# Optimization experiments

Measured on AMD Instinct MI355X. Metric: run time of the kernel, lower is better.

The kernel has to match this reference:

```python
import jax, jax.numpy as jnp
import numpy as np

B, L, C, H, D2 = 1, 384, 256, 8, 128
d = C // H
EPS = 1e-5
SCALE = 1.0 / np.sqrt(d).astype(np.float32)


def setup_inputs() -> dict:
    key = jax.random.key(0)
    ks = jax.random.split(key, 20)

    def lin(k, fin, fout):
        return (jax.random.normal(k, (fin, fout), jnp.float32) / np.sqrt(fin)).astype(jnp.float32)

    return {
        "x2d": jax.random.normal(ks[0], (B, L, L, D2), jnp.float32),
        "x3d": jax.random.normal(ks[1], (B, L, C), jnp.float32),
        "Wq": lin(ks[2], C, C), "bq": jax.random.normal(ks[3], (C,), jnp.float32) * 0.02,
        "Wk": lin(ks[4], C, C), "bk": jax.random.normal(ks[5], (C,), jnp.float32) * 0.02,
        "Wv": lin(ks[6], C, C), "bv": jax.random.normal(ks[7], (C,), jnp.float32) * 0.02,
        "Wpre": lin(ks[8], D2, C), "bpre": jax.random.normal(ks[9], (C,), jnp.float32) * 0.02,
        "ln_g": jnp.ones((C,), jnp.float32), "ln_b": jnp.zeros((C,), jnp.float32),
        "Weq": lin(ks[10], C, C), "beq": jax.random.normal(ks[11], (C,), jnp.float32) * 0.02,
        "Wek": lin(ks[12], C, C), "bek": jax.random.normal(ks[13], (C,), jnp.float32) * 0.02,
        "Wo": lin(ks[14], C, C), "bo": jax.random.normal(ks[15], (C,), jnp.float32) * 0.02,
    }


def reference(x2d, x3d, Wq, bq, Wk, bk, Wv, bv, Wpre, bpre, ln_g, ln_b,
              Weq, beq, Wek, bek, Wo, bo):
    def heads(x):  # (B,L,C) -> (B,H,L,d)
        return x.reshape(B, L, H, d).transpose(0, 2, 1, 3)

    q = heads(x3d @ Wq + bq)
    k = heads(x3d @ Wk + bk)
    v = heads(x3d @ Wv + bv)

    # pre_proj: Linear -> LayerNorm -> ReLU on pair features
    e = x2d @ Wpre + bpre                              # (B,L,L,C)
    mu = jnp.mean(e, axis=-1, keepdims=True)
    var = jnp.mean((e - mu) ** 2, axis=-1, keepdims=True)
    e = jax.nn.relu((e - mu) * jax.lax.rsqrt(var + EPS) * ln_g + ln_b)

    efq = (e @ Weq + beq).reshape(B, L, L, H, d)       # efq[b,i,j,h,:]
    efk = (e @ Wek + bek).reshape(B, L, L, H, d)

    # scores[b,h,i,j] = q_i.k_j + sum_d efk[b,i,j,h,d]*q[b,h,j,d], then scale
    scores = jnp.einsum('bhid,bhjd->bhij', q, k) \
           + jnp.einsum('bijhd,bhjd->bhij', efk, q)
    scores = scores * SCALE

    w = jax.nn.softmax(scores, axis=-1)
    x1 = jnp.einsum('bhij,bhjd->bhid', w, v)
    # x2[b,h,i,d] = sum_j scores[b,h,i,j] * efq[b,i,j,h,d]
    x2 = jnp.einsum('bhij,bijhd->bhid', scores, efq)

    x = (x1 + x2).transpose(0, 2, 1, 3).reshape(B, L, C)
    return x @ Wo + bo
```

## Files before the change

kernel.cpp:

```cpp
#include <hip/hip_runtime.h>
#include <hip/hip_bf16.h>

#define LLEN 384
#define CDIM 256
#define NH 8
#define HD 32
#define DIN 128
#define LN_EPS 1e-5f
#define SCL 0.17677669529663687f

#define EIDX(row, cs) (((row) << 8) + (((((cs) >> 3) ^ ((row) & 7)) << 3) | ((cs) & 4)))
#define XIDX(row, cs) (((row) << 7) + (((((cs) >> 3) ^ ((row) & 7)) << 3) | ((cs) & 4)))

typedef __attribute__((ext_vector_type(8))) short bh8;
typedef __attribute__((ext_vector_type(4))) float f32x4;
typedef __attribute__((ext_vector_type(4))) unsigned int u32x4;

__device__ __forceinline__ unsigned short f2bf(float f){
  unsigned int u = __float_as_uint(f);
  u += 0x7fffu + ((u >> 16) & 1u);
  return (unsigned short)(u >> 16);
}

__device__ __forceinline__ unsigned int pkbf(float a, float b){
#if defined(__gfx950__) && __has_builtin(__builtin_amdgcn_cvt_pk_bf16_f32)
  typedef __attribute__((ext_vector_type(2))) __bf16 vbf2;
  vbf2 v = __builtin_amdgcn_cvt_pk_bf16_f32(a, b);
  union { vbf2 v; unsigned int u; } cv; cv.v = v; return cv.u;
#else
  return (unsigned int)f2bf(a) | ((unsigned int)f2bf(b) << 16);
#endif
}

__global__ __launch_bounds__(256) void pack_w(
    const float* __restrict__ Wpre, const float* __restrict__ Weq,
    const float* __restrict__ Wek,  const float* __restrict__ Wq,
    const float* __restrict__ Wk,   const float* __restrict__ Wv,
    unsigned short* __restrict__ Pp, unsigned short* __restrict__ Pq,
    unsigned short* __restrict__ Pk, unsigned short* __restrict__ PWq,
    unsigned short* __restrict__ PWk, unsigned short* __restrict__ PWv)
{
  int tid = blockIdx.x * 256 + threadIdx.x;
  const float* W; unsigned short* P; int base;
  if      (tid <  4096){ W = Wpre; P = Pp;  base = tid;         }
  else if (tid < 12288){ W = Weq;  P = Pq;  base = tid -  4096; }
  else if (tid < 20480){ W = Wek;  P = Pk;  base = tid - 12288; }
  else if (tid < 28672){ W = Wq;   P = PWq; base = tid - 20480; }
  else if (tid < 36864){ W = Wk;   P = PWk; base = tid - 28672; }
  else                 { W = Wv;   P = PWv; base = tid - 36864; }
  int l   = base & 63;
  int c   = (base >> 6) & 15;
  int kc  = base >> 10;
  int krow = kc*32 + (l >> 4)*8;
  int col  = c*16 + (l & 15);
  unsigned int wds[4];
  #pragma unroll
  for (int p = 0; p < 4; p++){
    unsigned short lo = f2bf(W[(size_t)(krow + 2*p    )*CDIM + col]);
    unsigned short hi = f2bf(W[(size_t)(krow + 2*p + 1)*CDIM + col]);
    wds[p] = (unsigned int)lo | ((unsigned int)hi << 16);
  }
  uint4 v; v.x = wds[0]; v.y = wds[1]; v.z = wds[2]; v.w = wds[3];
  *(uint4*)(P + (size_t)base*8) = v;
}

__global__ __launch_bounds__(256) void qkv_mfma(
    const float* __restrict__ x3d,
    const float* __restrict__ bq, const float* __restrict__ bk, const float* __restrict__ bv,
    const unsigned short* __restrict__ PWq, const unsigned short* __restrict__ PWk,
    const unsigned short* __restrict__ PWv,
    float* __restrict__ Vm, unsigned short* __restrict__ QmH,
    float* __restrict__ QmT, unsigned short* __restrict__ PKt)
{
  __shared__ __align__(16) unsigned short Xb[64*264];
  const int bx = blockIdx.x;
  const int jb = bx / 3, m = bx % 3;
  const int t  = threadIdx.x;
  const int w  = t >> 6, l = t & 63, q4 = l >> 4, lm = l & 15;
  const int wbase = w << 6;

  const float* src = x3d + (size_t)jb*64*CDIM;
  #pragma unroll
  for (int it = 0; it < 16; it++){
    int idx = it*256 + t;
    int r = idx >> 6, k4 = (idx & 63) << 2;
    f32x4 v = *(const f32x4*)(src + (size_t)r*CDIM + k4);
    uint2 pk; pk.x = pkbf(v[0], v[1]); pk.y = pkbf(v[2], v[3]);
    *(uint2*)(&Xb[r*264 + k4]) = pk;
  }
  __syncthreads();

  const unsigned short* P = (m == 0) ? PWq : (m == 1) ? PWk : PWv;
  const float* bias       = (m == 0) ? bq  : (m == 1) ? bk  : bv;
  f32x4 acc[4][4];
  #pragma unroll
  for (int a = 0; a < 4; a++)
    #pragma unroll
    for (int b = 0; b < 4; b++){ f32x4 z = {0.f,0.f,0.f,0.f}; acc[a][b] = z; }
  #pragma unroll
  for (int kc = 0; kc < 8; kc++){
    bh8 af[4];
    #pragma unroll
    for (int rt = 0; rt < 4; rt++)
      af[rt] = *(const bh8*)(&Xb[(rt*16 + lm)*264 + kc*32 + q4*8]);
    #pragma unroll
    for (int ct = 0; ct < 4; ct++){
      bh8 bf = *(const bh8*)(P + ((size_t)(kc*16 + (w*4 + ct))*64 + l)*8);
      #pragma unroll
      for (int rt = 0; rt < 4; rt++)
        acc[rt][ct] = __builtin_amdgcn_mfma_f32_16x16x32_bf16(af[rt], bf, acc[rt][ct], 0, 0, 0);
    }
  }
  #pragma unroll
  for (int ct = 0; ct < 4; ct++){
    int c = wbase + ct*16 + lm;
    float bb = bias[c];
    #pragma unroll
    for (int rt = 0; rt < 4; rt++)
      #pragma unroll
      for (int rg = 0; rg < 4; rg++){
        int row = jb*64 + rt*16 + q4*4 + rg;
        float v = acc[rt][ct][rg] + bb;
        if (m == 0){
          QmH[(size_t)row*CDIM + c] = f2bf(v);
          QmT[(size_t)c*LLEN + row] = v;
        } else if (m == 1){
          int kc2 = c >> 5;
          int jj2 = c & 7;
          int l2  = ((c >> 3) & 3)*16 + (row & 15);
          PKt[(((size_t)kc2*24 + (row >> 4))*64 + l2)*8 + jj2] = f2bf(v);
        } else {
          Vm[(size_t)row*CDIM + c] = v;
        }
      }
  }
}

__global__ __launch_bounds__(256, 4) void x3d_tiles(
  const float* __restrict__ x2d,
  const float* __restrict__ bpre, const float* __restrict__ ln_g, const float* __restrict__ ln_b,
  const float* __restrict__ beq,  const float* __restrict__ bek,
  const float* __restrict__ QmT,  const unsigned short* __restrict__ QmH,
  const unsigned short* __restrict__ PKt,
  const unsigned short* __restrict__ Pp, const unsigned short* __restrict__ Pq,
  const unsigned short* __restrict__ Pk,
  float* __restrict__ Sg, float* __restrict__ x2part)
{
  __shared__ __align__(16) unsigned short EX[64*256];
  __shared__ float rowstat[4][64][2];
  __shared__ float muS[64], istdS[64];
  __shared__ __align__(16) float scoresS[NH*64];

  const int bx = blockIdx.x;
  const int i = bx / 6, jt = bx % 6, j0 = jt * 64;
  const int t = threadIdx.x;
  const int w = t >> 6, l = t & 63, q4 = l >> 4, lm = l & 15;
  const int wbase = w << 6;
  const bool b4 = l & 16, b5 = l & 32;

  #pragma unroll
  for (int hh = 0; hh < 2; hh++){
    int h = 2*w + hh;
    bh8 aq = *(const bh8*)(QmH + (size_t)i*CDIM + h*HD + q4*8);
    #pragma unroll
    for (int ct = 0; ct < 4; ct++){
      bh8 bf = *(const bh8*)(PKt + (((size_t)h*24 + (jt*4 + ct))*64 + l)*8);
      f32x4 z = {0.f,0.f,0.f,0.f};
      f32x4 a1 = __builtin_amdgcn_mfma_f32_16x16x32_bf16(aq, bf, z, 0, 0, 0);
      if (q4 == 0) scoresS[h*64 + ct*16 + lm] = a1[0];
    }
  }

  {
    const float* src = x2d + ((size_t)i*LLEN + j0)*DIN;
    #pragma unroll
    for (int it = 0; it < 8; it++){
      int r  = it*8 + (t >> 5);
      int k4 = (t & 31)*4;
      u32x4 uv = __builtin_nontemporal_load((const u32x4*)(src + (size_t)r*DIN + k4));
      uint2 pk;
      pk.x = pkbf(__uint_as_float(uv.x), __uint_as_float(uv.y));
      pk.y = pkbf(__uint_as_float(uv.z), __uint_as_float(uv.w));
      *(uint2*)(&EX[XIDX(r, k4)]) = pk;
    }
  }
  __syncthreads();

  f32x4 acc[4][4];
  #pragma unroll
  for (int a = 0; a < 4; a++)
    #pragma unroll
    for (int b = 0; b < 4; b++){ f32x4 z = {0.f,0.f,0.f,0.f}; acc[a][b] = z; }
  #pragma unroll
  for (int kc = 0; kc < 4; kc++){
    bh8 xf[4];
    #pragma unroll
    for (int nt = 0; nt < 4; nt++)
      xf[nt] = *(const bh8*)(&EX[XIDX(nt*16 + lm, kc*32 + q4*8)]);
    #pragma unroll
    for (int mt = 0; mt < 4; mt++){
      bh8 wf = *(const bh8*)(Pp + ((size_t)(kc*16 + (w*4 + mt))*64 + l)*8);
      #pragma unroll
      for (int nt = 0; nt < 4; nt++)
        acc[mt][nt] = __builtin_amdgcn_mfma_f32_16x16x32_bf16(wf, xf[nt], acc[mt][nt], 0, 0, 0);
    }
  }

  {
    float vs[4] = {0,0,0,0}, vq[4] = {0,0,0,0};
    #pragma unroll
    for (int mt = 0; mt < 4; mt++){
      int cb = wbase + mt*16 + q4*4;
      f32x4 bp = *(const f32x4*)(bpre + cb);
      #pragma unroll
      for (int nt = 0; nt < 4; nt++)
        #pragma unroll
        for (int rg = 0; rg < 4; rg++){
          float x = acc[mt][nt][rg] + bp[rg];
          acc[mt][nt][rg] = x;
          vs[nt] += x; vq[nt] += x*x;
        }
    }
    float r0 = (b4 ? vs[1] : vs[0]) + __shfl_xor(b4 ? vs[0] : vs[1], 16, 64);
    float r1 = (b4 ? vs[3] : vs[2]) + __shfl_xor(b4 ? vs[2] : vs[3], 16, 64);
    float ssum = (b5 ? r1 : r0) + __shfl_xor(b5 ? r0 : r1, 32, 64);
    float u0 = (b4 ? vq[1] : vq[0]) + __shfl_xor(b4 ? vq[0] : vq[1], 16, 64);
    float u1 = (b4 ? vq[3] : vq[2]) + __shfl_xor(b4 ? vq[2] : vq[3], 16, 64);
    float ssq = (b5 ? u1 : u0) + __shfl_xor(b5 ? u0 : u1, 32, 64);
    int ntl = (b5 ? 2 : 0) + (b4 ? 1 : 0);
    int jl = ntl*16 + lm;
    rowstat[w][jl][0] = ssum;
    rowstat[w][jl][1] = ssq;
  }
  __syncthreads();
  if (t < 64){
    float s  = rowstat[0][t][0] + rowstat[1][t][0] + rowstat[2][t][0] + rowstat[3][t][0];
    float s2 = rowstat[0][t][1] + rowstat[1][t][1] + rowstat[2][t][1] + rowstat[3][t][1];
    float mu = s * (1.f/256.f);
    float var = s2 * (1.f/256.f) - mu*mu;
    muS[t] = mu;
    istdS[t] = rsqrtf(var + LN_EPS);
  }
  __syncthreads();

  {
    float muL[4], isL[4];
    #pragma unroll
    for (int nt = 0; nt < 4; nt++){
      muL[nt] = muS[nt*16 + lm];
      isL[nt] = istdS[nt*16 + lm];
    }
    #pragma unroll
    for (int mt = 0; mt < 4; mt++){
      int cb = wbase + mt*16 + q4*4;
      f32x4 g4 = *(const f32x4*)(ln_g + cb);
      f32x4 bb4 = *(const f32x4*)(ln_b + cb);
      #pragma unroll
      for (int nt = 0; nt < 4; nt++){
        float e0 = fmaxf((acc[mt][nt][0] - muL[nt])*isL[nt]*g4[0] + bb4[0], 0.f);
        float e1 = fmaxf((acc[mt][nt][1] - muL[nt])*isL[nt]*g4[1] + bb4[1], 0.f);
        float e2 = fmaxf((acc[mt][nt][2] - muL[nt])*isL[nt]*g4[2] + bb4[2], 0.f);
        float e3 = fmaxf((acc[mt][nt][3] - muL[nt])*isL[nt]*g4[3] + bb4[3], 0.f);
        uint2 pk; pk.x = pkbf(e0, e1); pk.y = pkbf(e2, e3);
        *(uint2*)(&EX[EIDX(nt*16 + lm, cb)]) = pk;
      }
    }
  }
  __syncthreads();

  #pragma unroll
  for (int a = 0; a < 4; a++)
    #pragma unroll
    for (int b = 0; b < 4; b++){ f32x4 z = {0.f,0.f,0.f,0.f}; acc[a][b] = z; }
  #pragma unroll
  for (int kc = 0; kc < 8; kc++){
    bh8 xf[4];
    #pragma unroll
    for (int nt = 0; nt < 4; nt++)
      xf[nt] = *(const bh8*)(&EX[EIDX(nt*16 + lm, kc*32 + q4*8)]);
    #pragma unroll
    for (int mt = 0; mt < 4; mt++){
      bh8 wf = *(const bh8*)(Pk + ((size_t)(kc*16 + (w*4 + mt))*64 + l)*8);
      #pragma unroll
      for (int nt = 0; nt < 4; nt++)
        acc[mt][nt] = __builtin_amdgcn_mfma_f32_16x16x32_bf16(wf, xf[nt], acc[mt][nt], 0, 0, 0);
    }
  }

  {
    f32x4 bk4[4];
    #pragma unroll
    for (int mt = 0; mt < 4; mt++)
      bk4[mt] = *(const f32x4*)(bek + wbase + mt*16 + q4*4);
    #pragma unroll
    for (int nt = 0; nt < 4; nt++){
      int j = nt*16 + lm;
      float qr[4][4];
      #pragma unroll
      for (int mt = 0; mt < 4; mt++){
        int cb = wbase + mt*16 + q4*4;
        #pragma unroll
        for (int rg = 0; rg < 4; rg++)
          qr[mt][rg] = QmT[(size_t)(cb + rg)*LLEN + j0 + j];
      }
      float v0 = 0.f, v1 = 0.f;
      #pragma unroll
      for (int mt = 0; mt < 4; mt++){
        float p = (acc[mt][nt][0] + bk4[mt][0]) * qr[mt][0]
                + (acc[mt][nt][1] + bk4[mt][1]) * qr[mt][1]
                + (acc[mt][nt][2] + bk4[mt][2]) * qr[mt][2]
                + (acc[mt][nt][3] + bk4[mt][3]) * qr[mt][3];
        if (mt < 2) v0 += p; else v1 += p;
      }
      float r = (b4 ? v1 : v0) + __shfl_xor(b4 ? v0 : v1, 16, 64);
      float s = r + __shfl_xor(r, 32, 64);
      int h = 2*w + (b4 ? 1 : 0);
      float sc = (s + scoresS[h*64 + j]) * SCL;
      if (!b5){
        scoresS[h*64 + j] = sc;
        Sg[((size_t)i*NH + h)*LLEN + j0 + j] = sc;
      }
    }
  }

  #pragma unroll
  for (int a = 0; a < 4; a++)
    #pragma unroll
    for (int b = 0; b < 4; b++){ f32x4 z = {0.f,0.f,0.f,0.f}; acc[a][b] = z; }
  #pragma unroll
  for (int kc = 0; kc < 8; kc++){
    bh8 af[4];
    #pragma unroll
    for (int rt = 0; rt < 4; rt++)
      af[rt] = *(const bh8*)(&EX[EIDX(rt*16 + lm, kc*32 + q4*8)]);
    #pragma unroll
    for (int ct = 0; ct < 4; ct++){
      bh8 bf = *(const bh8*)(Pq + ((size_t)(kc*16 + (w*4 + ct))*64 + l)*8);
      #pragma unroll
      for (int rt = 0; rt < 4; rt++)
        acc[rt][ct] = __builtin_amdgcn_mfma_f32_16x16x32_bf16(af[rt], bf, acc[rt][ct], 0, 0, 0);
    }
  }

  {
    float bq4[4];
    #pragma unroll
    for (int ct = 0; ct < 4; ct++) bq4[ct] = beq[wbase + ct*16 + lm];
    float x2p[4] = {0.f, 0.f, 0.f, 0.f};
    #pragma unroll
    for (int rt = 0; rt < 4; rt++){
      f32x4 s0 = *(const f32x4*)(&scoresS[(2*w    )*64 + rt*16 + q4*4]);
      f32x4 s1 = *(const f32x4*)(&scoresS[(2*w + 1)*64 + rt*16 + q4*4]);
      #pragma unroll
      for (int ct = 0; ct < 4; ct++){
        const f32x4& sv = (ct < 2) ? s0 : s1;
        #pragma unroll
        for (int rg = 0; rg < 4; rg++)
          x2p[ct] = fmaf(sv[rg], acc[rt][ct][rg] + bq4[ct], x2p[ct]);
      }
    }
    float r0 = (b4 ? x2p[1] : x2p[0]) + __shfl_xor(b4 ? x2p[0] : x2p[1], 16, 64);
    float r1 = (b4 ? x2p[3] : x2p[2]) + __shfl_xor(b4 ? x2p[2] : x2p[3], 16, 64);
    float q  = (b5 ? r1 : r0) + __shfl_xor(b5 ? r0 : r1, 32, 64);
    int ctq = (b4 ? 1 : 0) | (b5 ? 2 : 0);
    x2part[((size_t)jt*LLEN + i)*CDIM + wbase + ctq*16 + lm] = q;
  }
}

__global__ __launch_bounds__(256) void finish(
    const float* __restrict__ Sg, const float* __restrict__ x2part,
    const float* __restrict__ Vm, const float* __restrict__ Wo,
    const float* __restrict__ bo, float* __restrict__ out)
{
  __shared__ float scoresS[NH*LLEN];
  __shared__ float xoutS[CDIM];
  const int i = blockIdx.x;
  const int t = threadIdx.x;

  #pragma unroll
  for (int it = 0; it < 3; it++)
    ((float4*)scoresS)[it*256 + t] = ((const float4*)(Sg + (size_t)i*NH*LLEN))[it*256 + t];
  __syncthreads();

  const int h = t >> 5;
  const int g32 = t & 31;
  float sv[12];
  float mx = -3.0e38f;
  #pragma unroll
  for (int it = 0; it < 12; it++){
    float s = scoresS[h*LLEN + it*32 + g32];
    sv[it] = s;
    mx = fmaxf(mx, s);
  }
  #pragma unroll
  for (int mk = 1; mk < 32; mk <<= 1) mx = fmaxf(mx, __shfl_xor(mx, mk, 64));
  float den = 0.f;
  #pragma unroll
  for (int it = 0; it < 12; it++){ float e = __expf(sv[it] - mx); sv[it] = e; den += e; }
  #pragma unroll
  for (int mk = 1; mk < 32; mk <<= 1) den += __shfl_xor(den, mk, 64);
  float rden = 1.f / den;
  #pragma unroll
  for (int it = 0; it < 12; it++) scoresS[h*LLEN + it*32 + g32] = sv[it]*rden;
  __syncthreads();

  float a0 = 0.f, a1 = 0.f, a2 = 0.f, a3 = 0.f;
  {
    const float* vp = Vm + t;
    const float* sp = scoresS + h*LLEN;
    #pragma unroll 4
    for (int j = 0; j < LLEN; j += 4){
      a0 = fmaf(sp[j+0], vp[(size_t)(j+0)*CDIM], a0);
      a1 = fmaf(sp[j+1], vp[(size_t)(j+1)*CDIM], a1);
      a2 = fmaf(sp[j+2], vp[(size_t)(j+2)*CDIM], a2);
      a3 = fmaf(sp[j+3], vp[(size_t)(j+3)*CDIM], a3);
    }
  }
  float x2v = 0.f;
  #pragma unroll
  for (int jt = 0; jt < 6; jt++)
    x2v += x2part[((size_t)jt*LLEN + i)*CDIM + t];
  xoutS[t] = (a0 + a1) + (a2 + a3) + x2v;
  __syncthreads();

  float b0a = bo[t], b1a = 0.f, b2a = 0.f, b3a = 0.f;
  #pragma unroll 4
  for (int c = 0; c < CDIM; c += 4){
    b0a = fmaf(xoutS[c+0], Wo[(size_t)(c+0)*CDIM + t], b0a);
    b1a = fmaf(xoutS[c+1], Wo[(size_t)(c+1)*CDIM + t], b1a);
    b2a = fmaf(xoutS[c+2], Wo[(size_t)(c+2)*CDIM + t], b2a);
    b3a = fmaf(xoutS[c+3], Wo[(size_t)(c+3)*CDIM + t], b3a);
  }
  out[(size_t)i*CDIM + t] = (b0a + b1a) + (b2a + b3a);
}

extern "C" void kernel_launch(void* const* d_in, const int* in_sizes, int n_in,
                              void* d_out, int out_size, void* d_ws, size_t ws_size,
                              hipStream_t stream)
{
  const float* x2d  = (const float*)d_in[0];
  const float* x3d  = (const float*)d_in[1];
  const float* Wq   = (const float*)d_in[2];
  const float* bq   = (const float*)d_in[3];
  const float* Wk   = (const float*)d_in[4];
  const float* bk   = (const float*)d_in[5];
  const float* Wv   = (const float*)d_in[6];
  const float* bv   = (const float*)d_in[7];
  const float* Wpre = (const float*)d_in[8];
  const float* bpre = (const float*)d_in[9];
  const float* ln_g = (const float*)d_in[10];
  const float* ln_b = (const float*)d_in[11];
  const float* Weq  = (const float*)d_in[12];
  const float* beq  = (const float*)d_in[13];
  const float* Wek  = (const float*)d_in[14];
  const float* bek  = (const float*)d_in[15];
  const float* Wo   = (const float*)d_in[16];
  const float* bo   = (const float*)d_in[17];
  float* out = (float*)d_out;

  float* Vm  = (float*)d_ws;
  float* QmT = Vm + LLEN*CDIM;
  unsigned short* QmH = (unsigned short*)(QmT + CDIM*LLEN);
  unsigned short* PKt = QmH + LLEN*CDIM;
  unsigned short* Pp  = PKt + LLEN*CDIM;
  unsigned short* Pq  = Pp  + DIN*CDIM;
  unsigned short* Pk  = Pq  + CDIM*CDIM;
  unsigned short* PWq = Pk  + CDIM*CDIM;
  unsigned short* PWk = PWq + CDIM*CDIM;
  unsigned short* PWv = PWk + CDIM*CDIM;
  float* Sg     = (float*)(PWv + CDIM*CDIM);
  float* x2part = Sg + (size_t)LLEN*NH*LLEN;

  pack_w<<<dim3(176), dim3(256), 0, stream>>>(Wpre, Weq, Wek, Wq, Wk, Wv,
                                              Pp, Pq, Pk, PWq, PWk, PWv);
  qkv_mfma<<<dim3(18), dim3(256), 0, stream>>>(x3d, bq, bk, bv, PWq, PWk, PWv,
                                               Vm, QmH, QmT, PKt);
  x3d_tiles<<<dim3(LLEN*6), dim3(256), 0, stream>>>(x2d, bpre, ln_g, ln_b, beq, bek,
                                                    QmT, QmH, PKt, Pp, Pq, Pk, Sg, x2part);
  finish<<<dim3(LLEN), dim3(256), 0, stream>>>(Sg, x2part, Vm, Wo, bo, out);
}
```

Measured before the change: 247.0 us.

## Loop three j-tiles per block with register prefetch of next x2d tile

The main tile kernel now processes three 64-column j-tiles per block (768 blocks instead of 2304). It prefetches the next x2d tile into registers while the current tile is computed, and x2 partials accumulate across the loop so only two partial rows per i reach the finish kernel. Separate LDS buffers for the input tile and the activated tile make the overlap possible. The cost is a larger LDS footprint, more registers from the prefetch buffer, and a lower launch-bounds occupancy hint (4 to 3), with fewer blocks left to fill the GPU.

```diff
diff --git a/kernel.cpp b/kernel.cpp
--- a/kernel.cpp
+++ b/kernel.cpp
@@ -136,7 +136,7 @@
   }
 }
 
-__global__ __launch_bounds__(256, 4) void x3d_tiles(
+__global__ __launch_bounds__(256, 3) void x3d_tiles(
   const float* __restrict__ x2d,
   const float* __restrict__ bpre, const float* __restrict__ ln_g, const float* __restrict__ ln_b,
   const float* __restrict__ beq,  const float* __restrict__ bek,
@@ -146,224 +146,244 @@
   const unsigned short* __restrict__ Pk,
   float* __restrict__ Sg, float* __restrict__ x2part)
 {
-  __shared__ __align__(16) unsigned short EX[64*256];
+  __shared__ __align__(16) unsigned short XS[64*128];
+  __shared__ __align__(16) unsigned short ES[64*256];
   __shared__ float rowstat[4][64][2];
   __shared__ float muS[64], istdS[64];
   __shared__ __align__(16) float scoresS[NH*64];
 
   const int bx = blockIdx.x;
-  const int i = bx / 6, jt = bx % 6, j0 = jt * 64;
+  const int i = bx >> 1, jh = bx & 1;
   const int t = threadIdx.x;
   const int w = t >> 6, l = t & 63, q4 = l >> 4, lm = l & 15;
   const int wbase = w << 6;
   const bool b4 = l & 16, b5 = l & 32;
-
-  #pragma unroll
-  for (int hh = 0; hh < 2; hh++){
-    int h = 2*w + hh;
-    bh8 aq = *(const bh8*)(QmH + (size_t)i*CDIM + h*HD + q4*8);
-    #pragma unroll
-    for (int ct = 0; ct < 4; ct++){
-      bh8 bf = *(const bh8*)(PKt + (((size_t)h*24 + (jt*4 + ct))*64 + l)*8);
-      f32x4 z = {0.f,0.f,0.f,0.f};
-      f32x4 a1 = __builtin_amdgcn_mfma_f32_16x16x32_bf16(aq, bf, z, 0, 0, 0);
-      if (q4 == 0) scoresS[h*64 + ct*16 + lm] = a1[0];
-    }
-  }
-
+  const int pr  = (t >> 5);
+  const int pk4 = (t & 31) * 4;
+
+  float x2p[4] = {0.f, 0.f, 0.f, 0.f};
+
+  u32x4 pf[8];
   {
-    const float* src = x2d + ((size_t)i*LLEN + j0)*DIN;
+    const float* src = x2d + ((size_t)i*LLEN + jh*192)*DIN;
+    #pragma unroll
+    for (int it = 0; it < 8; it++)
+      pf[it] = __builtin_nontemporal_load((const u32x4*)(src + (size_t)(it*8 + pr)*DIN + pk4));
+  }
+
+  for (int tt = 0; tt < 3; tt++){
+    const int j0 = jh*192 + tt*64;
+    const int jt = jh*3 + tt;
+
     #pragma unroll
     for (int it = 0; it < 8; it++){
-      int r  = it*8 + (t >> 5);
-      int k4 = (t & 31)*4;
-      u32x4 uv = __builtin_nontemporal_load((const u32x4*)(src + (size_t)r*DIN + k4));
-      uint2 pk;
-      pk.x = pkbf(__uint_as_float(uv.x), __uint_as_float(uv.y));
-      pk.y = pkbf(__uint_as_float(uv.z), __uint_as_float(uv.w));
-      *(uint2*)(&EX[XIDX(r, k4)]) = pk;
-    }
-  }
-  __syncthreads();
-
-  f32x4 acc[4][4];
-  #pragma unroll
-  for (int a = 0; a < 4; a++)
-    #pragma unroll
-    for (int b = 0; b < 4; b++){ f32x4 z = {0.f,0.f,0.f,0.f}; acc[a][b] = z; }
-  #pragma unroll
-  for (int kc = 0; kc < 4; kc++){
-    bh8 xf[4];
-    #pragma unroll
-    for (int nt = 0; nt < 4; nt++)
-      xf[nt] = *(const bh8*)(&EX[XIDX(nt*16 + lm, kc*32 + q4*8)]);
-    #pragma unroll
-    for (int mt = 0; mt < 4; mt++){
-      bh8 wf = *(const bh8*)(Pp + ((size_t)(kc*16 + (w*4 + mt))*64 + l)*8);
+      uint2 pkv;
+      pkv.x = pkbf(__uint_as_float(pf[it].x), __uint_as_float(pf[it].y));
+      pkv.y = pkbf(__uint_as_float(pf[it].z), __uint_as_float(pf[it].w));
+      *(uint2*)(&XS[XIDX(it*8 + pr, pk4)]) = pkv;
+    }
+    if (tt < 2){
+      const float* src = x2d + ((size_t)i*LLEN + j0 + 64)*DIN;
+      #pragma unroll
+      for (int it = 0; it < 8; it++)
+        pf[it] = __builtin_nontemporal_load((const u32x4*)(src + (size_t)(it*8 + pr)*DIN + pk4));
+    }
+
+    #pragma unroll
+    for (int hh = 0; hh < 2; hh++){
+      int h = 2*w + hh;
+      bh8 aq = *(const bh8*)(QmH + (size_t)i*CDIM + h*HD + q4*8);
+      #pragma unroll
+      for (int ct = 0; ct < 4; ct++){
+        bh8 bf = *(const bh8*)(PKt + (((size_t)h*24 + (jt*4 + ct))*64 + l)*8);
+        f32x4 z = {0.f,0.f,0.f,0.f};
+        f32x4 a1 = __builtin_amdgcn_mfma_f32_16x16x32_bf16(aq, bf, z, 0, 0, 0);
+        if (q4 == 0) scoresS[h*64 + ct*16 + lm] = a1[0];
+      }
+    }
+    __syncthreads();
+
+    f32x4 acc[4][4];
+    #pragma unroll
+    for (int a = 0; a < 4; a++)
+      #pragma unroll
+      for (int b = 0; b < 4; b++){ f32x4 z = {0.f,0.f,0.f,0.f}; acc[a][b] = z; }
+    #pragma unroll
+    for (int kc = 0; kc < 4; kc++){
+      bh8 xf[4];
       #pragma unroll
       for (int nt = 0; nt < 4; nt++)
-        acc[mt][nt] = __builtin_amdgcn_mfma_f32_16x16x32_bf16(wf, xf[nt], acc[mt][nt], 0, 0, 0);
-    }
-  }
-
-  {
-    float vs[4] = {0,0,0,0}, vq[4] = {0,0,0,0};
-    #pragma unroll
-    for (int mt = 0; mt < 4; mt++){
-      int cb = wbase + mt*16 + q4*4;
-      f32x4 bp = *(const f32x4*)(bpre + cb);
-      #pragma unroll
-      for (int nt = 0; nt < 4; nt++)
-        #pragma unroll
-        for (int rg = 0; rg < 4; rg++){
-          float x = acc[mt][nt][rg] + bp[rg];
-          acc[mt][nt][rg] = x;
-          vs[nt] += x; vq[nt] += x*x;
-        }
-    }
-    float r0 = (b4 ? vs[1] : vs[0]) + __shfl_xor(b4 ? vs[0] : vs[1], 16, 64);
-    float r1 = (b4 ? vs[3] : vs[2]) + __shfl_xor(b4 ? vs[2] : vs[3], 16, 64);
-    float ssum = (b5 ? r1 : r0) + __shfl_xor(b5 ? r0 : r1, 32, 64);
-    float u0 = (b4 ? vq[1] : vq[0]) + __shfl_xor(b4 ? vq[0] : vq[1], 16, 64);
-    float u1 = (b4 ? vq[3] : vq[2]) + __shfl_xor(b4 ? vq[2] : vq[3], 16, 64);
-    float ssq = (b5 ? u1 : u0) + __shfl_xor(b5 ? u0 : u1, 32, 64);
-    int ntl = (b5 ? 2 : 0) + (b4 ? 1 : 0);
-    int jl = ntl*16 + lm;
-    rowstat[w][jl][0] = ssum;
-    rowstat[w][jl][1] = ssq;
-  }
-  __syncthreads();
-  if (t < 64){
-    float s  = rowstat[0][t][0] + rowstat[1][t][0] + rowstat[2][t][0] + rowstat[3][t][0];
-    float s2 = rowstat[0][t][1] + rowstat[1][t][1] + rowstat[2][t][1] + rowstat[3][t][1];
-    float mu = s * (1.f/256.f);
-    float var = s2 * (1.f/256.f) - mu*mu;
-    muS[t] = mu;
-    istdS[t] = rsqrtf(var + LN_EPS);
-  }
-  __syncthreads();
-
-  {
-    float muL[4], isL[4];
-    #pragma unroll
-    for (int nt = 0; nt < 4; nt++){
-      muL[nt] = muS[nt*16 + lm];
-      isL[nt] = istdS[nt*16 + lm];
-    }
-    #pragma unroll
-    for (int mt = 0; mt < 4; mt++){
-      int cb = wbase + mt*16 + q4*4;
-      f32x4 g4 = *(const f32x4*)(ln_g + cb);
-      f32x4 bb4 = *(const f32x4*)(ln_b + cb);
-      #pragma unroll
-      for (int nt = 0; nt < 4; nt++){
-        float e0 = fmaxf((acc[mt][nt][0] - muL[nt])*isL[nt]*g4[0] + bb4[0], 0.f);
-        float e1 = fmaxf((acc[mt][nt][1] - muL[nt])*isL[nt]*g4[1] + bb4[1], 0.f);
-        float e2 = fmaxf((acc[mt][nt][2] - muL[nt])*isL[nt]*g4[2] + bb4[2], 0.f);
-        float e3 = fmaxf((acc[mt][nt][3] - muL[nt])*isL[nt]*g4[3] + bb4[3], 0.f);
-        uint2 pk; pk.x = pkbf(e0, e1); pk.y = pkbf(e2, e3);
-        *(uint2*)(&EX[EIDX(nt*16 + lm, cb)]) = pk;
-      }
-    }
-  }
-  __syncthreads();
-
-  #pragma unroll
-  for (int a = 0; a < 4; a++)
-    #pragma unroll
-    for (int b = 0; b < 4; b++){ f32x4 z = {0.f,0.f,0.f,0.f}; acc[a][b] = z; }
-  #pragma unroll
-  for (int kc = 0; kc < 8; kc++){
-    bh8 xf[4];
-    #pragma unroll
-    for (int nt = 0; nt < 4; nt++)
-      xf[nt] = *(const bh8*)(&EX[EIDX(nt*16 + lm, kc*32 + q4*8)]);
-    #pragma unroll
-    for (int mt = 0; mt < 4; mt++){
-      bh8 wf = *(const bh8*)(Pk + ((size_t)(kc*16 + (w*4 + mt))*64 + l)*8);
-      #pragma unroll
-      for (int nt = 0; nt < 4; nt++)
-        acc[mt][nt] = __builtin_amdgcn_mfma_f32_16x16x32_bf16(wf, xf[nt], acc[mt][nt], 0, 0, 0);
-    }
-  }
-
-  {
-    f32x4 bk4[4];
-    #pragma unroll
-    for (int mt = 0; mt < 4; mt++)
-      bk4[mt] = *(const f32x4*)(bek + wbase + mt*16 + q4*4);
-    #pragma unroll
-    for (int nt = 0; nt < 4; nt++){
-      int j = nt*16 + lm;
-      float qr[4][4];
+        xf[nt] = *(const bh8*)(&XS[XIDX(nt*16 + lm, kc*32 + q4*8)]);
+      #pragma unroll
+      for (int mt = 0; mt < 4; mt++){
+        bh8 wf = *(const bh8*)(Pp + ((size_t)(kc*16 + (w*4 + mt))*64 + l)*8);
+        #pragma unroll
+        for (int nt = 0; nt < 4; nt++)
+          acc[mt][nt] = __builtin_amdgcn_mfma_f32_16x16x32_bf16(wf, xf[nt], acc[mt][nt], 0, 0, 0);
+      }
+    }
+
+    {
+      float vs[4] = {0,0,0,0}, vq[4] = {0,0,0,0};
       #pragma unroll
       for (int mt = 0; mt < 4; mt++){
         int cb = wbase + mt*16 + q4*4;
-        #pragma unroll
-        for (int rg = 0; rg < 4; rg++)
-          qr[mt][rg] = QmT[(size_t)(cb + rg)*LLEN + j0 + j];
-      }
-      float v0 = 0.f, v1 = 0.f;
+        f32x4 bp = *(const f32x4*)(bpre + cb);
+        #pragma unroll
+        for (int nt = 0; nt < 4; nt++)
+          #pragma unroll
+          for (int rg = 0; rg < 4; rg++){
+            float x = acc[mt][nt][rg] + bp[rg];
+            acc[mt][nt][rg] = x;
+            vs[nt] += x; vq[nt] += x*x;
+          }
+      }
+      float r0 = (b4 ? vs[1] : vs[0]) + __shfl_xor(b4 ? vs[0] : vs[1], 16, 64);
+      float r1 = (b4 ? vs[3] : vs[2]) + __shfl_xor(b4 ? vs[2] : vs[3], 16, 64);
+      float ssum = (b5 ? r1 : r0) + __shfl_xor(b5 ? r0 : r1, 32, 64);
+      float u0 = (b4 ? vq[1] : vq[0]) + __shfl_xor(b4 ? vq[0] : vq[1], 16, 64);
+      float u1 = (b4 ? vq[3] : vq[2]) + __shfl_xor(b4 ? vq[2] : vq[3], 16, 64);
+      float ssq = (b5 ? u1 : u0) + __shfl_xor(b5 ? u0 : u1, 32, 64);
+      int ntl = (b5 ? 2 : 0) + (b4 ? 1 : 0);
+      int jl = ntl*16 + lm;
+      rowstat[w][jl][0] = ssum;
+      rowstat[w][jl][1] = ssq;
+    }
+    __syncthreads();
+    if (t < 64){
+      float s  = rowstat[0][t][0] + rowstat[1][t][0] + rowstat[2][t][0] + rowstat[3][t][0];
+      float s2 = rowstat[0][t][1] + rowstat[1][t][1] + rowstat[2][t][1] + rowstat[3][t][1];
+      float mu = s * (1.f/256.f);
+      float var = s2 * (1.f/256.f) - mu*mu;
+      muS[t] = mu;
+      istdS[t] = rsqrtf(var + LN_EPS);
+    }
+    __syncthreads();
+
+    {
+      float muL[4], isL[4];
+      #pragma unroll
+      for (int nt = 0; nt < 4; nt++){
+        muL[nt] = muS[nt*16 + lm];
+        isL[nt] = istdS[nt*16 + lm];
+      }
       #pragma unroll
       for (int mt = 0; mt < 4; mt++){
-        float p = (acc[mt][nt][0] + bk4[mt][0]) * qr[mt][0]
-                + (acc[mt][nt][1] + bk4[mt][1]) * qr[mt][1]
-                + (acc[mt][nt][2] + bk4[mt][2]) * qr[mt][2]
-                + (acc[mt][nt][3] + bk4[mt][3]) * qr[mt][3];
-        if (mt < 2) v0 += p; else v1 += p;
-      }
-      float r = (b4 ? v1 : v0) + __shfl_xor(b4 ? v0 : v1, 16, 64);
-      float s = r + __shfl_xor(r, 32, 64);
-      int h = 2*w + (b4 ? 1 : 0);
-      float sc = (s + scoresS[h*64 + j]) * SCL;
-      if (!b5){
-        scoresS[h*64 + j] = sc;
-        Sg[((size_t)i*NH + h)*LLEN + j0 + j] = sc;
-      }
-    }
-  }
-
-  #pragma unroll
-  for (int a = 0; a < 4; a++)
-    #pragma unroll
-    for (int b = 0; b < 4; b++){ f32x4 z = {0.f,0.f,0.f,0.f}; acc[a][b] = z; }
-  #pragma unroll
-  for (int kc = 0; kc < 8; kc++){
-    bh8 af[4];
-    #pragma unroll
-    for (int rt = 0; rt < 4; rt++)
-      af[rt] = *(const bh8*)(&EX[EIDX(rt*16 + lm, kc*32 + q4*8)]);
-    #pragma unroll
-    for (int ct = 0; ct < 4; ct++){
-      bh8 bf = *(const bh8*)(Pq + ((size_t)(kc*16 + (w*4 + ct))*64 + l)*8);
+        int cb = wbase + mt*16 + q4*4;
+        f32x4 g4 = *(const f32x4*)(ln_g + cb);
+        f32x4 bb4 = *(const f32x4*)(ln_b + cb);
+        #pragma unroll
+        for (int nt = 0; nt < 4; nt++){
+          float e0 = fmaxf((acc[mt][nt][0] - muL[nt])*isL[nt]*g4[0] + bb4[0], 0.f);
+          float e1 = fmaxf((acc[mt][nt][1] - muL[nt])*isL[nt]*g4[1] + bb4[1], 0.f);
+          float e2 = fmaxf((acc[mt][nt][2] - muL[nt])*isL[nt]*g4[2] + bb4[2], 0.f);
+          float e3 = fmaxf((acc[mt][nt][3] - muL[nt])*isL[nt]*g4[3] + bb4[3], 0.f);
+          uint2 pkv; pkv.x = pkbf(e0, e1); pkv.y = pkbf(e2, e3);
+          *(uint2*)(&ES[EIDX(nt*16 + lm, cb)]) = pkv;
+        }
+      }
+    }
+    __syncthreads();
+
+    #pragma unroll
+    for (int a = 0; a < 4; a++)
+      #pragma unroll
+      for (int b = 0; b < 4; b++){ f32x4 z = {0.f,0.f,0.f,0.f}; acc[a][b] = z; }
+    #pragma unroll
+    for (int kc = 0; kc < 8; kc++){
+      bh8 xf[4];
+      #pragma unroll
+      for (int nt = 0; nt < 4; nt++)
+        xf[nt] = *(const bh8*)(&ES[EIDX(nt*16 + lm, kc*32 + q4*8)]);
+      #pragma unroll
+      for (int mt = 0; mt < 4; mt++){
+        bh8 wf = *(const bh8*)(Pk + ((size_t)(kc*16 + (w*4 + mt))*64 + l)*8);
+        #pragma unroll
+        for (int nt = 0; nt < 4; nt++)
+          acc[mt][nt] = __builtin_amdgcn_mfma_f32_16x16x32_bf16(wf, xf[nt], acc[mt][nt], 0, 0, 0);
+      }
+    }
+
+    {
+      f32x4 bk4[4];
+      #pragma unroll
+      for (int mt = 0; mt < 4; mt++)
+        bk4[mt] = *(const f32x4*)(bek + wbase + mt*16 + q4*4);
+      #pragma unroll
+      for (int nt = 0; nt < 4; nt++){
+        int j = nt*16 + lm;
+        float qr[4][4];
+        #pragma unroll
+        for (int mt = 0; mt < 4; mt++){
+          int cb = wbase + mt*16 + q4*4;
+          #pragma unroll
+          for (int rg = 0; rg < 4; rg++)
+            qr[mt][rg] = QmT[(size_t)(cb + rg)*LLEN + j0 + j];
+        }
+        float v0 = 0.f, v1 = 0.f;
+        #pragma unroll
+        for (int mt = 0; mt < 4; mt++){
+          float p = (acc[mt][nt][0] + bk4[mt][0]) * qr[mt][0]
+                  + (acc[mt][nt][1] + bk4[mt][1]) * qr[mt][1]
+                  + (acc[mt][nt][2] + bk4[mt][2]) * qr[mt][2]
+                  + (acc[mt][nt][3] + bk4[mt][3]) * qr[mt][3];
+          if (mt < 2) v0 += p; else v1 += p;
+        }
+        float r = (b4 ? v1 : v0) + __shfl_xor(b4 ? v0 : v1, 16, 64);
+        float s = r + __shfl_xor(r, 32, 64);
+        int h = 2*w + (b4 ? 1 : 0);
+        float sc = (s + scoresS[h*64 + j]) * SCL;
+        if (!b5){
+          scoresS[h*64 + j] = sc;
+          Sg[((size_t)i*NH + h)*LLEN + j0 + j] = sc;
+        }
+      }
+    }
+
+    #pragma unroll
+    for (int a = 0; a < 4; a++)
+      #pragma unroll
+      for (int b = 0; b < 4; b++){ f32x4 z = {0.f,0.f,0.f,0.f}; acc[a][b] = z; }
+    #pragma unroll
+    for (int kc = 0; kc < 8; kc++){
+      bh8 af[4];
       #pragma unroll
       for (int rt = 0; rt < 4; rt++)
-        acc[rt][ct] = __builtin_amdgcn_mfma_f32_16x16x32_bf16(af[rt], bf, acc[rt][ct], 0, 0, 0);
+        af[rt] = *(const bh8*)(&ES[EIDX(rt*16 + lm, kc*32 + q4*8)]);
+      #pragma unroll
+      for (int ct = 0; ct < 4; ct++){
+        bh8 bf = *(const bh8*)(Pq + ((size_t)(kc*16 + (w*4 + ct))*64 + l)*8);
+        #pragma unroll
+        for (int rt = 0; rt < 4; rt++)
+          acc[rt][ct] = __builtin_amdgcn_mfma_f32_16x16x32_bf16(af[rt], bf, acc[rt][ct], 0, 0, 0);
+      }
+    }
+
+    {
+      float bq4[4];
+      #pragma unroll
+      for (int ct = 0; ct < 4; ct++) bq4[ct] = beq[wbase + ct*16 + lm];
+      #pragma unroll
+      for (int rt = 0; rt < 4; rt++){
+        f32x4 s0 = *(const f32x4*)(&scoresS[(2*w    )*64 + rt*16 + q4*4]);
+        f32x4 s1 = *(const f32x4*)(&scoresS[(2*w + 1)*64 + rt*16 + q4*4]);
+        #pragma unroll
+        for (int ct = 0; ct < 4; ct++){
+          const f32x4& sv = (ct < 2) ? s0 : s1;
+          #pragma unroll
+          for (int rg = 0; rg < 4; rg++)
+            x2p[ct] = fmaf(sv[rg], acc[rt][ct][rg] + bq4[ct], x2p[ct]);
+        }
+      }
     }
   }
 
   {
-    float bq4[4];
-    #pragma unroll
-    for (int ct = 0; ct < 4; ct++) bq4[ct] = beq[wbase + ct*16 + lm];
-    float x2p[4] = {0.f, 0.f, 0.f, 0.f};
-    #pragma unroll
-    for (int rt = 0; rt < 4; rt++){
-      f32x4 s0 = *(const f32x4*)(&scoresS[(2*w    )*64 + rt*16 + q4*4]);
-      f32x4 s1 = *(const f32x4*)(&scoresS[(2*w + 1)*64 + rt*16 + q4*4]);
-      #pragma unroll
-      for (int ct = 0; ct < 4; ct++){
-        const f32x4& sv = (ct < 2) ? s0 : s1;
-        #pragma unroll
-        for (int rg = 0; rg < 4; rg++)
-          x2p[ct] = fmaf(sv[rg], acc[rt][ct][rg] + bq4[ct], x2p[ct]);
-      }
-    }
     float r0 = (b4 ? x2p[1] : x2p[0]) + __shfl_xor(b4 ? x2p[0] : x2p[1], 16, 64);
     float r1 = (b4 ? x2p[3] : x2p[2]) + __shfl_xor(b4 ? x2p[2] : x2p[3], 16, 64);
     float q  = (b5 ? r1 : r0) + __shfl_xor(b5 ? r0 : r1, 32, 64);
     int ctq = (b4 ? 1 : 0) | (b5 ? 2 : 0);
-    x2part[((size_t)jt*LLEN + i)*CDIM + wbase + ctq*16 + lm] = q;
+    x2part[((size_t)jh*LLEN + i)*CDIM + wbase + ctq*16 + lm] = q;
   }
 }
 
@@ -416,10 +436,7 @@
       a3 = fmaf(sp[j+3], vp[(size_t)(j+3)*CDIM], a3);
     }
   }
-  float x2v = 0.f;
-  #pragma unroll
-  for (int jt = 0; jt < 6; jt++)
-    x2v += x2part[((size_t)jt*LLEN + i)*CDIM + t];
+  float x2v = x2part[(size_t)i*CDIM + t] + x2part[((size_t)LLEN + i)*CDIM + t];
   xoutS[t] = (a0 + a1) + (a2 + a3) + x2v;
   __syncthreads();
 
@@ -475,7 +492,7 @@
                                               Pp, Pq, Pk, PWq, PWk, PWv);
   qkv_mfma<<<dim3(18), dim3(256), 0, stream>>>(x3d, bq, bk, bv, PWq, PWk, PWv,
                                                Vm, QmH, QmT, PKt);
-  x3d_tiles<<<dim3(LLEN*6), dim3(256), 0, stream>>>(x2d, bpre, ln_g, ln_b, beq, bek,
+  x3d_tiles<<<dim3(LLEN*2), dim3(256), 0, stream>>>(x2d, bpre, ln_g, ln_b, beq, bek,
                                                     QmT, QmH, PKt, Pp, Pq, Pk, Sg, x2part);
   finish<<<dim3(LLEN), dim3(256), 0, stream>>>(Sg, x2part, Vm, Wo, bo, out);
 }
```

After: 534.4 us. 116% more time.
